# Kernel optimization log

Hardware: AMD Instinct MI355X
Metric: run time of the kernel (lower is better)

## Reference

```python
import jax, jax.numpy as jnp
import numpy as np

EPS = 1e-5

def _normalize(v):
    # F.normalize(v, p=2, dim=-1, eps=1e-5): v / max(||v||_2, eps)
    n = jnp.sqrt(jnp.sum(v * v, axis=-1, keepdims=True))
    return v / jnp.maximum(n, EPS)

def setup_inputs() -> dict:
    key = jax.random.key(0)
    kx, ke = jax.random.split(key)
    B, T, C, K = 16, 2048, 512, 1024
    x = jax.random.normal(kx, (B, T, C), dtype=jnp.float32)
    emb = jax.random.normal(ke, (K, C), dtype=jnp.float32)  # embedding.weight
    return {"x": x, "emb": emb}

def reference(x, emb):
    B, T, C = x.shape
    # Squared distances (argmin of cdist == argmin of squared distance):
    x2 = jnp.sum(x * x, axis=-1, keepdims=True)          # [B,T,1]
    e2 = jnp.sum(emb * emb, axis=-1)                      # [K]
    xe = jnp.einsum('btc,kc->btk', x, emb)                # [B,T,K]
    dist2 = x2 - 2.0 * xe + e2                            # [B,T,K]
    idx = jnp.argmin(dist2, axis=-1)                      # [B,T] int
    quant = jnp.take(emb, idx, axis=0)                    # [B,T,C]
    x_norm = _normalize(x)
    q_norm = _normalize(quant)
    commitment_loss = jnp.mean((jax.lax.stop_gradient(q_norm) - x_norm) ** 2, axis=(1, 2))  # [B]
    codebook_loss = jnp.mean((q_norm - jax.lax.stop_gradient(x_norm)) ** 2, axis=(1, 2))    # [B]
    # Straight-through estimator
    quant_out = x + jax.lax.stop_gradient(quant - x)
    return quant_out, codebook_loss, commitment_loss, idx
```

## Files before the change

### kernel.cpp

```cpp
#include <hip/hip_runtime.h>

typedef unsigned short u16;
typedef unsigned int u32;
typedef _Float16 half8 __attribute__((ext_vector_type(8)));
typedef float f32x4 __attribute__((ext_vector_type(4)));

#define BT    32768
#define CD    512
#define KC    1024
#define LOFF1 16777216
#define LOFF2 16777232
#define IOFF  16777248

#define WS_EH   0
#define WS_E2   1048576
#define WS_KW   1052672
#define WS_PART 1183744

static __device__ __forceinline__ u16 f2h(float f) {
  union { _Float16 h; u16 u; } c;
  c.h = (_Float16)f;
  return c.u;
}

static __device__ __forceinline__ void gload16(const void* g, void* l) {
  __builtin_amdgcn_global_load_lds(
      (const __attribute__((address_space(1))) u32*)g,
      (__attribute__((address_space(3))) u32*)l, 16, 0, 0);
}

__global__ __launch_bounds__(256) void convx_kernel(const float4* __restrict__ x4,
                                                    uint2* __restrict__ xh2) {
  const int i = blockIdx.x * 256 + threadIdx.x;
  const float4 v = x4[i];
  uint2 o;
  o.x = (u32)f2h(v.x) | ((u32)f2h(v.y) << 16);
  o.y = (u32)f2h(v.z) | ((u32)f2h(v.w) << 16);
  xh2[i] = o;
}

__global__ __launch_bounds__(256) void conve_kernel(const float* __restrict__ emb,
                                                    u16* __restrict__ eh,
                                                    float* __restrict__ e2) {
  const int lane = threadIdx.x & 63;
  const int r    = blockIdx.x * 4 + (threadIdx.x >> 6);
  const float4* er = reinterpret_cast<const float4*>(emb + (size_t)r * CD);
  const float4 a = er[lane*2], b = er[lane*2+1];
  uint4 o;
  o.x = (u32)f2h(a.x) | ((u32)f2h(a.y) << 16);
  o.y = (u32)f2h(a.z) | ((u32)f2h(a.w) << 16);
  o.z = (u32)f2h(b.x) | ((u32)f2h(b.y) << 16);
  o.w = (u32)f2h(b.z) | ((u32)f2h(b.w) << 16);
  reinterpret_cast<uint4*>(eh + (size_t)r * CD)[lane] = o;
  float s = a.x*a.x + a.y*a.y + a.z*a.z + a.w*a.w
          + b.x*b.x + b.y*b.y + b.z*b.z + b.w*b.w;
  for (int off = 32; off > 0; off >>= 1) s += __shfl_down(s, off, 64);
  if (lane == 0) e2[r] = s;
}

__global__ __launch_bounds__(256) void mfma_argmin_kernel(
    const u16* __restrict__ xh, const u16* __restrict__ eh,
    const float* __restrict__ e2, const float* __restrict__ x,
    const float* __restrict__ emb, float* __restrict__ out,
    int* __restrict__ kwin, float* __restrict__ part) {
  __shared__ __align__(16) char smem[38400];
  u16*   sA   = (u16*)smem;
  u16*   sB   = (u16*)(smem + 4096);
  float* e2s  = (float*)(smem + 20480);
  u32*   cand = (u32*)smem;
  int*   top4k = (int*)(smem + 32768);
  double* dref = (double*)(smem + 33792);
  float* q2a  = (float*)(smem + 35840);
  float* xqa  = (float*)(smem + 36864);
  float* x2a  = (float*)(smem + 37888);

  const int tid  = threadIdx.x;
  const int wv   = tid >> 6;
  const int lane = tid & 63;
  const int lm   = lane & 15;
  const int lq   = lane >> 4;
  const int m0   = blockIdx.x * 64;

  u32 t0[16], t1[16];
#pragma unroll
  for (int s = 0; s < 16; ++s) { t0[s] = 0xFFFFFFFFu; t1[s] = 0xFFFFFFFFu; }

  const u16* gA = xh + (size_t)(m0 + wv*16 + lm) * CD + lq*8;

  for (int nt = 0; nt < 4; ++nt) {
    __syncthreads();
    e2s[tid] = e2[nt*256 + tid];

    f32x4 acc[4][4];
#pragma unroll
    for (int i = 0; i < 4; ++i)
#pragma unroll
      for (int j = 0; j < 4; ++j)
        acc[i][j] = (f32x4){0.f, 0.f, 0.f, 0.f};

    for (int ks = 0; ks < 16; ++ks) {
      __syncthreads();
      gload16(gA + ks*32, sA + wv*512);
#pragma unroll
      for (int tjl = 0; tjl < 4; ++tjl) {
        const u16* gB = eh + (size_t)(nt*256 + wv*64 + tjl*16 + lm) * CD + ks*32 + lq*8;
        gload16(gB, sB + (wv*4 + tjl)*512);
      }
      __syncthreads();
      half8 bf[4];
#pragma unroll
      for (int tjl = 0; tjl < 4; ++tjl)
        bf[tjl] = *(const half8*)(sB + (wv*4 + tjl)*512 + lane*8);
#pragma unroll
      for (int ti = 0; ti < 4; ++ti) {
        const half8 af = *(const half8*)(sA + ti*512 + lane*8);
#pragma unroll
        for (int tjl = 0; tjl < 4; ++tjl)
          acc[ti][tjl] = __builtin_amdgcn_mfma_f32_16x16x32_f16(
              af, bf[tjl], acc[ti][tjl], 0, 0, 0);
      }
    }

#pragma unroll
    for (int tjl = 0; tjl < 4; ++tjl) {
      const float ek = e2s[wv*64 + tjl*16 + lm];
      const u32 col  = (u32)(nt*256 + wv*64 + tjl*16 + lm);
#pragma unroll
      for (int ti = 0; ti < 4; ++ti)
#pragma unroll
        for (int reg = 0; reg < 4; ++reg) {
          const float d = ek - 2.f * acc[ti][tjl][reg] + 1024.f;
          const u32 p = (__float_as_uint(d) & 0xFFFFFC00u) | col;
          const int s = ti*4 + reg;
          if (p < t0[s]) { t1[s] = t0[s]; t0[s] = p; }
          else if (p < t1[s]) { t1[s] = p; }
        }
    }
  }

  __syncthreads();
#pragma unroll
  for (int s = 0; s < 16; ++s) {
    const int ti = s >> 2, reg = s & 3;
    const int row = ti*16 + lq*4 + reg;
    uint2 pr; pr.x = t0[s]; pr.y = t1[s];
    *reinterpret_cast<uint2*>(&cand[row*128 + wv*32 + lm*2]) = pr;
  }
  __syncthreads();

  if (tid < 64) {
    u32 u0 = 0xFFFFFFFFu, u1 = 0xFFFFFFFFu, u2 = 0xFFFFFFFFu, u3 = 0xFFFFFFFFu;
    for (int i = 0; i < 128; ++i) {
      const u32 v = cand[tid*128 + ((i + tid*2) & 127)];
      if (v < u3) {
        if (v < u2) {
          u3 = u2;
          if (v < u1) {
            u2 = u1;
            if (v < u0) { u1 = u0; u0 = v; } else { u1 = v; }
          } else { u2 = v; }
        } else { u3 = v; }
      }
    }
    top4k[tid*4+0] = (int)(u0 & 1023u);
    top4k[tid*4+1] = (int)(u1 & 1023u);
    top4k[tid*4+2] = (int)(u2 & 1023u);
    top4k[tid*4+3] = (int)(u3 & 1023u);
  }
  __syncthreads();

  {
    const int rr = tid >> 2, cc = tid & 3;
    const int k = top4k[rr*4 + cc];
    const float4* xr = reinterpret_cast<const float4*>(x   + (size_t)(m0+rr) * CD);
    const float4* er = reinterpret_cast<const float4*>(emb + (size_t)k * CD);
    double d0 = 0.0, d1 = 0.0;
    float q2 = 0.f, xq = 0.f, x2 = 0.f;
    for (int i = 0; i < CD/4; ++i) {
      const float4 a = xr[i], b = er[i];
      const double ta = (double)a.x - (double)b.x;
      const double tb = (double)a.y - (double)b.y;
      const double tc = (double)a.z - (double)b.z;
      const double td = (double)a.w - (double)b.w;
      d0 += ta*ta + tc*tc;
      d1 += tb*tb + td*td;
      q2 += b.x*b.x + b.y*b.y + b.z*b.z + b.w*b.w;
      xq += a.x*b.x + a.y*b.y + a.z*b.z + a.w*b.w;
      x2 += a.x*a.x + a.y*a.y + a.z*a.z + a.w*a.w;
    }
    dref[rr*4 + cc] = d0 + d1;
    q2a[rr*4 + cc] = q2;
    xqa[rr*4 + cc] = xq;
    if (cc == 0) x2a[rr] = x2;
  }
  __syncthreads();

  if (tid < 64) {
    double bd = dref[tid*4]; int bk = top4k[tid*4]; int bc = 0;
#pragma unroll
    for (int c = 1; c < 4; ++c) {
      const double dc = dref[tid*4 + c];
      const int kc = top4k[tid*4 + c];
      if (dc < bd || (dc == bd && kc < bk)) { bd = dc; bk = kc; bc = c; }
    }
    const int gr = m0 + tid;
    out[IOFF + gr] = (float)bk;
    kwin[gr] = bk;

    const float q2 = q2a[tid*4 + bc];
    const float xq = xqa[tid*4 + bc];
    const float x2 = x2a[tid];
    const float nx = fmaxf(sqrtf(x2), 1e-5f);
    const float nq = fmaxf(sqrtf(q2), 1e-5f);
    float s = q2/(nq*nq) + x2/(nx*nx) - 2.f*xq/(nx*nq);
    for (int off = 32; off > 0; off >>= 1) s += __shfl_down(s, off, 64);
    if (tid == 0) part[blockIdx.x] = s;
  }
}

__global__ __launch_bounds__(256) void gather_kernel(
    const float* __restrict__ emb, const int* __restrict__ kwin,
    float* __restrict__ out) {
  const int lane = threadIdx.x & 63;
  const int r    = blockIdx.x * 4 + (threadIdx.x >> 6);
  const int k    = kwin[r] & (KC - 1);
  const float4* er = reinterpret_cast<const float4*>(emb + (size_t)k * CD);
  float4* qr = reinterpret_cast<float4*>(out + (size_t)r * CD);
  qr[lane*2]   = er[lane*2];
  qr[lane*2+1] = er[lane*2+1];
}

__global__ void loss_write_kernel(const float* __restrict__ part,
                                  float* __restrict__ out) {
  const int t = threadIdx.x;
  if (t < 16) {
    float acc = 0.f;
    for (int i = 0; i < 32; ++i) acc += part[32*t + i];
    const float v = acc * (1.f / 1048576.f);
    out[LOFF1 + t] = v;
    out[LOFF2 + t] = v;
  }
}

extern "C" void kernel_launch(void* const* d_in, const int* in_sizes, int n_in,
                              void* d_out, int out_size, void* d_ws, size_t ws_size,
                              hipStream_t stream) {
  const float* x   = (const float*)d_in[0];
  const float* emb = (const float*)d_in[1];
  float* out = (float*)d_out;

  u16*   eh   = (u16*)((char*)d_ws + WS_EH);
  float* e2   = (float*)((char*)d_ws + WS_E2);
  int*   kwin = (int*)((char*)d_ws + WS_KW);
  float* part = (float*)((char*)d_ws + WS_PART);
  u16*   xh   = (u16*)out;

  convx_kernel<<<BT * CD / 4 / 256, 256, 0, stream>>>(
      (const float4*)x, (uint2*)xh);
  conve_kernel<<<KC / 4, 256, 0, stream>>>(emb, eh, e2);
  mfma_argmin_kernel<<<BT / 64, 256, 0, stream>>>(
      xh, eh, e2, x, emb, out, kwin, part);
  gather_kernel<<<BT / 4, 256, 0, stream>>>(emb, kwin, out);
  loss_write_kernel<<<1, 64, 0, stream>>>(part, out);
}
```

Before: 257.1 us.

## Fuse x conversion and gather into argmin kernel with register-prefetched B

Drops the separate fp32-to-fp16 conversion pass over x and the separate gather kernel. Each block now converts its 64 rows of x straight into LDS, keeping the whole A tile (64 KB) resident. It reads codebook fragments directly from global memory into registers with double-buffered prefetch, so the per-k-step __syncthreads go away, and it writes the quantized rows at the end. The cost is about 70 KB of LDS per block, which lowers occupancy, and codebook loads are no longer staged through LDS, so there is no sharing across waves.

```diff
diff --git a/kernel.cpp b/kernel.cpp
--- a/kernel.cpp
+++ b/kernel.cpp
@@ -14,29 +14,12 @@
 
 #define WS_EH   0
 #define WS_E2   1048576
-#define WS_KW   1052672
-#define WS_PART 1183744
+#define WS_PART 1052672
 
 static __device__ __forceinline__ u16 f2h(float f) {
   union { _Float16 h; u16 u; } c;
   c.h = (_Float16)f;
   return c.u;
-}
-
-static __device__ __forceinline__ void gload16(const void* g, void* l) {
-  __builtin_amdgcn_global_load_lds(
-      (const __attribute__((address_space(1))) u32*)g,
-      (__attribute__((address_space(3))) u32*)l, 16, 0, 0);
-}
-
-__global__ __launch_bounds__(256) void convx_kernel(const float4* __restrict__ x4,
-                                                    uint2* __restrict__ xh2) {
-  const int i = blockIdx.x * 256 + threadIdx.x;
-  const float4 v = x4[i];
-  uint2 o;
-  o.x = (u32)f2h(v.x) | ((u32)f2h(v.y) << 16);
-  o.y = (u32)f2h(v.z) | ((u32)f2h(v.w) << 16);
-  xh2[i] = o;
 }
 
 __global__ __launch_bounds__(256) void conve_kernel(const float* __restrict__ emb,
@@ -58,21 +41,20 @@
   if (lane == 0) e2[r] = s;
 }
 
-__global__ __launch_bounds__(256) void mfma_argmin_kernel(
-    const u16* __restrict__ xh, const u16* __restrict__ eh,
-    const float* __restrict__ e2, const float* __restrict__ x,
-    const float* __restrict__ emb, float* __restrict__ out,
-    int* __restrict__ kwin, float* __restrict__ part) {
-  __shared__ __align__(16) char smem[38400];
-  u16*   sA   = (u16*)smem;
-  u16*   sB   = (u16*)(smem + 4096);
-  float* e2s  = (float*)(smem + 20480);
-  u32*   cand = (u32*)smem;
-  int*   top4k = (int*)(smem + 32768);
-  double* dref = (double*)(smem + 33792);
-  float* q2a  = (float*)(smem + 35840);
-  float* xqa  = (float*)(smem + 36864);
-  float* x2a  = (float*)(smem + 37888);
+__global__ __launch_bounds__(256) void mfma_fused_kernel(
+    const u16* __restrict__ eh, const float* __restrict__ e2,
+    const float* __restrict__ x, const float* __restrict__ emb,
+    float* __restrict__ out, float* __restrict__ part) {
+  __shared__ __align__(16) char smem[70144];
+  u16*    sA    = (u16*)smem;
+  float*  e2s   = (float*)(smem + 65536);
+  int*    win   = (int*)(smem + 69632);
+  u32*    cand  = (u32*)smem;
+  int*    top4k = (int*)(smem + 32768);
+  double* dref  = (double*)(smem + 33792);
+  float*  q2a   = (float*)(smem + 35840);
+  float*  xqa   = (float*)(smem + 36864);
+  float*  x2a   = (float*)(smem + 37888);
 
   const int tid  = threadIdx.x;
   const int wv   = tid >> 6;
@@ -81,62 +63,96 @@
   const int lq   = lane >> 4;
   const int m0   = blockIdx.x * 64;
 
+  {
+    const float* xb = x + (size_t)m0 * CD;
+    const int tl = tid & 15;
+    const int tc = tid >> 4;
+#pragma unroll 8
+    for (int i = 0; i < 32; ++i) {
+      const int r  = (i & 3) * 16 + tl;
+      const int c4 = tc * 8 + (i >> 2);
+      const float4 v = *(const float4*)(xb + (size_t)r * CD + c4 * 4);
+      const int ks  = c4 >> 3;
+      const int lqw = (c4 >> 1) & 3;
+      const int j   = (c4 & 1) << 2;
+      const int ti  = r >> 4, lmw = r & 15;
+      uint2 o;
+      o.x = (u32)f2h(v.x) | ((u32)f2h(v.y) << 16);
+      o.y = (u32)f2h(v.z) | ((u32)f2h(v.w) << 16);
+      *(uint2*)(sA + ((ti*16 + ks) << 9) + ((lqw << 4) + lmw) * 8 + j) = o;
+    }
+    e2s[tid]       = e2[tid];
+    e2s[tid + 256] = e2[tid + 256];
+    e2s[tid + 512] = e2[tid + 512];
+    e2s[tid + 768] = e2[tid + 768];
+  }
+  __syncthreads();
+
+  f32x4 acc[4][4];
+#pragma unroll
+  for (int i = 0; i < 4; ++i)
+#pragma unroll
+    for (int j = 0; j < 4; ++j)
+      acc[i][j] = (f32x4){0.f, 0.f, 0.f, 0.f};
+
   u32 t0[16], t1[16];
 #pragma unroll
   for (int s = 0; s < 16; ++s) { t0[s] = 0xFFFFFFFFu; t1[s] = 0xFFFFFFFFu; }
 
-  const u16* gA = xh + (size_t)(m0 + wv*16 + lm) * CD + lq*8;
-
-  for (int nt = 0; nt < 4; ++nt) {
-    __syncthreads();
-    e2s[tid] = e2[nt*256 + tid];
-
-    f32x4 acc[4][4];
-#pragma unroll
-    for (int i = 0; i < 4; ++i)
-#pragma unroll
-      for (int j = 0; j < 4; ++j)
-        acc[i][j] = (f32x4){0.f, 0.f, 0.f, 0.f};
-
-    for (int ks = 0; ks < 16; ++ks) {
-      __syncthreads();
-      gload16(gA + ks*32, sA + wv*512);
-#pragma unroll
-      for (int tjl = 0; tjl < 4; ++tjl) {
-        const u16* gB = eh + (size_t)(nt*256 + wv*64 + tjl*16 + lm) * CD + ks*32 + lq*8;
-        gload16(gB, sB + (wv*4 + tjl)*512);
-      }
-      __syncthreads();
-      half8 bf[4];
-#pragma unroll
-      for (int tjl = 0; tjl < 4; ++tjl)
-        bf[tjl] = *(const half8*)(sB + (wv*4 + tjl)*512 + lane*8);
-#pragma unroll
-      for (int ti = 0; ti < 4; ++ti) {
-        const half8 af = *(const half8*)(sA + ti*512 + lane*8);
-#pragma unroll
-        for (int tjl = 0; tjl < 4; ++tjl)
-          acc[ti][tjl] = __builtin_amdgcn_mfma_f32_16x16x32_f16(
-              af, bf[tjl], acc[ti][tjl], 0, 0, 0);
-      }
-    }
-
-#pragma unroll
-    for (int tjl = 0; tjl < 4; ++tjl) {
-      const float ek = e2s[wv*64 + tjl*16 + lm];
-      const u32 col  = (u32)(nt*256 + wv*64 + tjl*16 + lm);
-#pragma unroll
-      for (int ti = 0; ti < 4; ++ti)
-#pragma unroll
-        for (int reg = 0; reg < 4; ++reg) {
-          const float d = ek - 2.f * acc[ti][tjl][reg] + 1024.f;
-          const u32 p = (__float_as_uint(d) & 0xFFFFFC00u) | col;
-          const int s = ti*4 + reg;
-          if (p < t0[s]) { t1[s] = t0[s]; t0[s] = p; }
-          else if (p < t1[s]) { t1[s] = p; }
-        }
-    }
-  }
+  const u16* eB = eh + (size_t)(wv*64 + lm) * CD + lq*8;
+
+  half8 afA[4], afB[4], bfA[4], bfB[4];
+
+#define PREF(IT, AF, BF) do {                                        \
+    const int nt_ = (IT) >> 4, ks_ = (IT) & 15;                      \
+    const u16* pb_ = eB + nt_ * 131072 + ks_ * 32;                   \
+    BF[0] = *(const half8*)(pb_);                                    \
+    BF[1] = *(const half8*)(pb_ + 8192);                             \
+    BF[2] = *(const half8*)(pb_ + 16384);                            \
+    BF[3] = *(const half8*)(pb_ + 24576);                            \
+    const u16* pa_ = sA + ks_ * 512 + lane * 8;                      \
+    AF[0] = *(const half8*)(pa_);                                    \
+    AF[1] = *(const half8*)(pa_ + 8192);                             \
+    AF[2] = *(const half8*)(pa_ + 16384);                            \
+    AF[3] = *(const half8*)(pa_ + 24576);                            \
+  } while (0)
+
+#define MM(AF, BF) do {                                              \
+    _Pragma("unroll") for (int ti_ = 0; ti_ < 4; ++ti_)              \
+      _Pragma("unroll") for (int tj_ = 0; tj_ < 4; ++tj_)            \
+        acc[ti_][tj_] = __builtin_amdgcn_mfma_f32_16x16x32_f16(      \
+            AF[ti_], BF[tj_], acc[ti_][tj_], 0, 0, 0);               \
+  } while (0)
+
+#define FOLD(NT) do {                                                \
+    _Pragma("unroll") for (int tj_ = 0; tj_ < 4; ++tj_) {            \
+      const int col_ = (NT)*256 + wv*64 + tj_*16 + lm;               \
+      const float ek_ = e2s[col_];                                   \
+      _Pragma("unroll") for (int ti_ = 0; ti_ < 4; ++ti_)            \
+        _Pragma("unroll") for (int rg_ = 0; rg_ < 4; ++rg_) {        \
+          const float d_ = ek_ - 2.f * acc[ti_][tj_][rg_] + 1024.f;  \
+          const u32 p_ = (__float_as_uint(d_) & 0xFFFFFC00u) | (u32)col_; \
+          const int s_ = ti_*4 + rg_;                                \
+          if (p_ < t0[s_]) { t1[s_] = t0[s_]; t0[s_] = p_; }         \
+          else if (p_ < t1[s_]) { t1[s_] = p_; }                     \
+          acc[ti_][tj_][rg_] = 0.f;                                  \
+        }                                                            \
+    }                                                                \
+  } while (0)
+
+  PREF(0, afA, bfA);
+#pragma unroll 1
+  for (int itp = 0; itp < 32; ++itp) {
+    const int it = itp << 1;
+    PREF(it + 1, afB, bfB);
+    MM(afA, bfA);
+    if (itp != 31) PREF(it + 2, afA, bfA);
+    MM(afB, bfB);
+    if ((itp & 7) == 7) FOLD(itp >> 3);
+  }
+#undef PREF
+#undef MM
+#undef FOLD
 
   __syncthreads();
 #pragma unroll
@@ -205,7 +221,7 @@
     }
     const int gr = m0 + tid;
     out[IOFF + gr] = (float)bk;
-    kwin[gr] = bk;
+    win[tid] = bk;
 
     const float q2 = q2a[tid*4 + bc];
     const float xq = xqa[tid*4 + bc];
@@ -216,18 +232,18 @@
     for (int off = 32; off > 0; off >>= 1) s += __shfl_down(s, off, 64);
     if (tid == 0) part[blockIdx.x] = s;
   }
-}
-
-__global__ __launch_bounds__(256) void gather_kernel(
-    const float* __restrict__ emb, const int* __restrict__ kwin,
-    float* __restrict__ out) {
-  const int lane = threadIdx.x & 63;
-  const int r    = blockIdx.x * 4 + (threadIdx.x >> 6);
-  const int k    = kwin[r] & (KC - 1);
-  const float4* er = reinterpret_cast<const float4*>(emb + (size_t)k * CD);
-  float4* qr = reinterpret_cast<float4*>(out + (size_t)r * CD);
-  qr[lane*2]   = er[lane*2];
-  qr[lane*2+1] = er[lane*2+1];
+  __syncthreads();
+
+  {
+    const float4* e4 = reinterpret_cast<const float4*>(emb);
+    float4* ob = reinterpret_cast<float4*>(out + (size_t)m0 * CD);
+#pragma unroll 8
+    for (int i = 0; i < 32; ++i) {
+      const int f = tid + (i << 8);
+      const int k = win[f >> 7];
+      ob[f] = e4[k*128 + (f & 127)];
+    }
+  }
 }
 
 __global__ void loss_write_kernel(const float* __restrict__ part,
@@ -251,15 +267,9 @@
 
   u16*   eh   = (u16*)((char*)d_ws + WS_EH);
   float* e2   = (float*)((char*)d_ws + WS_E2);
-  int*   kwin = (int*)((char*)d_ws + WS_KW);
   float* part = (float*)((char*)d_ws + WS_PART);
-  u16*   xh   = (u16*)out;
-
-  convx_kernel<<<BT * CD / 4 / 256, 256, 0, stream>>>(
-      (const float4*)x, (uint2*)xh);
+
   conve_kernel<<<KC / 4, 256, 0, stream>>>(emb, eh, e2);
-  mfma_argmin_kernel<<<BT / 64, 256, 0, stream>>>(
-      xh, eh, e2, x, emb, out, kwin, part);
-  gather_kernel<<<BT / 4, 256, 0, stream>>>(emb, kwin, out);
+  mfma_fused_kernel<<<BT / 64, 256, 0, stream>>>(eh, e2, x, emb, out, part);
   loss_write_kernel<<<1, 64, 0, stream>>>(part, out);
 }
```

Measured after the change: 238.6 us. -7.2%, faster.
